# Performance work log

Hardware: AMD Instinct MI355X
Metric: run time of the kernel (lower is better)

## Reference

```python
import math
import jax, jax.numpy as jnp
import numpy as np


def _skew(X, pad_value):
    # shift every row i one step right relative to row i-1: [B,M,L] -> [B,M,M+L]
    B, M, L = X.shape
    X = jnp.pad(X, ((0, 0), (0, 0), (0, M + 1)), constant_values=pad_value)
    X = X.reshape(B, -1)[:, :-M]
    return X.reshape(B, M, M + L)


def _unskew(X):
    # reverse of _skew: [B,M,M+L] -> [B,M,L]
    B, M, ML = X.shape
    L = ML - M
    X = X.reshape(B, -1)
    X = jnp.pad(X, ((0, 0), (0, M)))
    X = X.reshape(B, M, M + L + 1)
    return X[:, :, :L]


def setup_inputs() -> dict:
    key0 = jax.random.key(0)
    k1, k2, k3, k4 = jax.random.split(key0, 4)
    BH, M, D = 64, 1024, 64          # batch*heads, block len, head dim
    L = 1024                          # attn_span
    return {
        "query": jax.random.normal(k1, (BH, M, D), dtype=jnp.float32),
        "key": jax.random.normal(k2, (BH, M + L, D), dtype=jnp.float32),
        "value": jax.random.normal(k3, (BH, M + L, D), dtype=jnp.float32),
        "key_pe": jax.random.normal(k4, (1, D, L), dtype=jnp.float32),
    }


def reference(query, key, value, key_pe):
    hidden_size = query.shape[-1]
    # content scores: [BH, M, M+L] -> banded [BH, M, L]
    attn_cont = _unskew(jnp.matmul(query, jnp.swapaxes(key, -1, -2)))
    # relative position scores: [BH, M, L] (key_pe broadcasts over batch)
    attn_pos = jnp.matmul(query, key_pe)
    attn = (attn_cont + attn_pos) / math.sqrt(hidden_size)
    attn = jax.nn.softmax(attn, axis=-1)
    # dropout p=0.0 -> identity
    attn_skew = _skew(attn, 0.0)          # [BH, M, M+L]
    out = jnp.matmul(attn_skew, value)    # [BH, M, D]
    return out
```

## Files before the change

kernel.cpp:

```cpp
#include <hip/hip_runtime.h>
#include <hip/hip_bf16.h>


typedef __attribute__((ext_vector_type(8))) short bf16x8;
typedef __attribute__((ext_vector_type(4))) short bf16x4;
typedef __attribute__((ext_vector_type(4))) float f32x4;

#define BHN   64
#define MQ    1024
#define DH    64
#define LS    1024
#define NKEY  2048
#define NTILE 17

#define SZ_PE  ((size_t)LS * DH * 2)
#define OFF_K  SZ_PE
#define SZ_K   ((size_t)BHN * NKEY * DH * 2)
#define OFF_V  (OFF_K + SZ_K)
#define SZ_V   ((size_t)BHN * DH * NKEY * 2)
#define WS_NEED (OFF_V + SZ_V)

#define SCL_LOG2E 0.18033688011112042f

__device__ __forceinline__ short f2bf(float f) {
  unsigned u = __float_as_uint(f);
  u += 0x7FFFu + ((u >> 16) & 1u);
  return (short)(u >> 16);
}
__device__ __forceinline__ float bf2f(short s) {
  return __uint_as_float(((unsigned)(unsigned short)s) << 16);
}

#if defined(__has_builtin)
#if __has_builtin(__builtin_amdgcn_cvt_pk_bf16_f32)
#define HAVE_CVT_PK 1
#endif
#if __has_builtin(__builtin_amdgcn_exp2f)
#define HAVE_EXP2 1
#endif
#endif

__device__ __forceinline__ float fast_exp2(float x) {
#ifdef HAVE_EXP2
  return __builtin_amdgcn_exp2f(x);
#else
  return __builtin_exp2f(x);
#endif
}

__device__ __forceinline__ unsigned pk2c(float a, float b) {
  return (unsigned)(unsigned short)f2bf(a) | ((unsigned)(unsigned short)f2bf(b) << 16);
}

__device__ __forceinline__ unsigned pk2a(float a, float b) {
#ifdef HAVE_CVT_PK
  auto r = __builtin_amdgcn_cvt_pk_bf16_f32(a, b);
  unsigned u;
  __builtin_memcpy(&u, &r, 4);
  return u;
#else
  unsigned r;
  asm("v_cvt_pk_bf16_f32 %0, %1, %2" : "=v"(r) : "v"(a), "v"(b));
  return r;
#endif
}
__device__ __forceinline__ bf16x4 mk4(unsigned a, unsigned b) {
  union { unsigned u[2]; bf16x4 v; } z;
  z.u[0] = a; z.u[1] = b;
  return z.v;
}
__device__ __forceinline__ bf16x8 mk8(unsigned a, unsigned b, unsigned c, unsigned d) {
  union { unsigned u[4]; bf16x8 v; } z;
  z.u[0] = a; z.u[1] = b; z.u[2] = c; z.u[3] = d;
  return z.v;
}

__global__ __launch_bounds__(256)
void prep_fused(const float* __restrict__ pe, const float* __restrict__ K,
                const float* __restrict__ V, short* __restrict__ peT,
                short* __restrict__ Kb, short* __restrict__ Vb) {
  __shared__ short st[64 * 68];
  const int bx = blockIdx.x;
  if (bx < 256) {
    const int idx = bx * 256 + threadIdx.x;
    const int rel = idx >> 6, d = idx & 63;
    peT[rel * 64 + (((d >> 3) ^ (rel & 7)) * 8) + (d & 7)] = f2bf(pe[d * LS + rel]);
  } else if (bx < 2304) {
    const size_t i = ((size_t)(bx - 256) * 256 + threadIdx.x) * 16;
    const int row = (int)(i >> 6);
    const int c16 = (int)(i & 63);
    const float4 f0 = *(const float4*)(K + i);
    const float4 f1 = *(const float4*)(K + i + 4);
    const float4 f2 = *(const float4*)(K + i + 8);
    const float4 f3 = *(const float4*)(K + i + 12);
    const bf16x8 b0 = mk8(pk2c(f0.x, f0.y), pk2c(f0.z, f0.w), pk2c(f1.x, f1.y), pk2c(f1.z, f1.w));
    const bf16x8 b1 = mk8(pk2c(f2.x, f2.y), pk2c(f2.z, f2.w), pk2c(f3.x, f3.y), pk2c(f3.z, f3.w));
    const int s7 = row & 7;
    short* dst = Kb + (size_t)row * 64;
    *(bf16x8*)&dst[(((c16 >> 3))     ^ s7) * 8] = b0;
    *(bf16x8*)&dst[(((c16 >> 3) + 1) ^ s7) * 8] = b1;
  } else {
    const int b  = bx - 2304;
    const int bh = b >> 5, jt = b & 31;
    {
      const int r = threadIdx.x >> 2, cb = (threadIdx.x & 3) * 16;
      const float* src = V + ((size_t)bh * NKEY + jt * 64 + r) * DH + cb;
#pragma unroll
      for (int c = 0; c < 16; c += 8) {
        float4 f0 = *(const float4*)(src + c);
        float4 f1 = *(const float4*)(src + c + 4);
        *(bf16x8*)&st[r * 68 + cb + c] =
            mk8(pk2c(f0.x, f0.y), pk2c(f0.z, f0.w), pk2c(f1.x, f1.y), pk2c(f1.z, f1.w));
      }
    }
    __syncthreads();
    {
      const int d = threadIdx.x >> 2, kapb = (threadIdx.x & 3) * 16;
      __attribute__((aligned(16))) short tmp[16];
#pragma unroll
      for (int j = 0; j < 16; ++j) {
        const int kap = kapb + j;
        const int k   = (kap & 3) * 16 + (kap >> 2);
        tmp[j] = st[k * 68 + d];
      }
      short* dst = Vb + ((size_t)bh * DH + d) * NKEY + jt * 64 + kapb;
      *(bf16x8*)dst       = *(bf16x8*)&tmp[0];
      *(bf16x8*)(dst + 8) = *(bf16x8*)&tmp[8];
    }
  }
}

template <bool PRECONV>
__global__ __launch_bounds__(256, 4)
void seq_attn_kernel(const float* __restrict__ Qf, const float* __restrict__ Kf,
                     const float* __restrict__ Vf, const short* __restrict__ peT,
                     const short* __restrict__ Kb, const short* __restrict__ Vb,
                     float* __restrict__ Out) {
  __shared__ short sK[64 * 64];
  __shared__ short sPE[2 * 64 * 64];
  __shared__ short sV[64 * 64];

  const int tid  = threadIdx.x;
  const int w    = tid >> 6;
  const int lane = tid & 63;
  const int li   = lane & 15;
  const int quad = lane >> 4;
  const int linear = blockIdx.y * 16 + blockIdx.x;
  const int slot   = linear >> 3;
  const int bh     = (linear & 7) * 8 + (slot >> 4);
  const int i0     = (slot & 15) * 64;
  const int rbase  = w * 16 + quad * 4;

  bf16x8 aq[2];
  {
    const float* qp = Qf + (size_t)((bh * MQ + i0 + w * 16 + li) * DH) + quad * 8;
#pragma unroll
    for (int ks = 0; ks < 2; ++ks) {
      float4 f0 = *(const float4*)(qp + ks * 32);
      float4 f1 = *(const float4*)(qp + ks * 32 + 4);
      f0.x *= SCL_LOG2E; f0.y *= SCL_LOG2E; f0.z *= SCL_LOG2E; f0.w *= SCL_LOG2E;
      f1.x *= SCL_LOG2E; f1.y *= SCL_LOG2E; f1.z *= SCL_LOG2E; f1.w *= SCL_LOG2E;
      aq[ks] = mk8(pk2a(f0.x, f0.y), pk2a(f0.z, f0.w), pk2a(f1.x, f1.y), pk2a(f1.z, f1.w));
    }
  }

  float l_i[4] = {0.f, 0.f, 0.f, 0.f};
  f32x4 acco[4];
#pragma unroll
  for (int nt = 0; nt < 4; ++nt) acco[nt] = (f32x4){0.f, 0.f, 0.f, 0.f};

  f32x4 curPw[4];
  f32x4 prevw3 = (f32x4){0.f, 0.f, 0.f, 0.f};

  bf16x8 pfK0, pfK1, pfP0, pfP1, pfV0, pfV1;
  const short *pK, *pP, *pV0, *pV1;
  if constexpr (PRECONV) {
    pK = Kb + ((size_t)bh * NKEY + i0) * DH + tid * 8 + 1024;
    pP = peT + tid * 8 + 1024;
    const int d0 = tid >> 3;
    const int g0 = (tid & 7) ^ (d0 & 7);
    pV0 = Vb + ((size_t)bh * DH + d0) * NKEY + i0 + g0 * 8;
    pV1 = pV0 + (size_t)32 * NKEY;
    pfK0 = *(const bf16x8*)(pK - 1024);
    pfK1 = *(const bf16x8*)(pK + 1024);
    pfP0 = *(const bf16x8*)(pP - 1024);
    pfP1 = *(const bf16x8*)(pP + 1024);
    pfV0 = *(const bf16x8*)(pV0);
    pfV1 = *(const bf16x8*)(pV1);
    pK += 4096; pP += 4096; pV0 += 64; pV1 += 64;
  }

  for (int t = 0; t < NTILE; ++t) {
    if constexpr (PRECONV) {
      asm volatile("s_waitcnt lgkmcnt(0)" ::: "memory");
      __builtin_amdgcn_sched_barrier(0);
      __builtin_amdgcn_s_barrier();
      __builtin_amdgcn_sched_barrier(0);
      *(bf16x8*)&sK[tid * 8]        = pfK0;
      *(bf16x8*)&sK[tid * 8 + 2048] = pfK1;
      if (t < NTILE - 1) {
        short* ped = sPE + (size_t)(t & 1) * 4096;
        *(bf16x8*)&ped[tid * 8]        = pfP0;
        *(bf16x8*)&ped[tid * 8 + 2048] = pfP1;
      }
      *(bf16x8*)&sV[tid * 8]        = pfV0;
      *(bf16x8*)&sV[tid * 8 + 2048] = pfV1;
      if (t + 1 < NTILE) {
        pfK0 = *(const bf16x8*)(pK - 1024);
        pfK1 = *(const bf16x8*)(pK + 1024);
        pfV0 = *(const bf16x8*)(pV0);
        pfV1 = *(const bf16x8*)(pV1);
        pK += 4096; pV0 += 64; pV1 += 64;
        if (t + 1 < NTILE - 1) {
          pfP0 = *(const bf16x8*)(pP - 1024);
          pfP1 = *(const bf16x8*)(pP + 1024);
          pP += 4096;
        }
      }
      asm volatile("s_waitcnt lgkmcnt(0)" ::: "memory");
      __builtin_amdgcn_sched_barrier(0);
      __builtin_amdgcn_s_barrier();
      __builtin_amdgcn_sched_barrier(0);
    } else {
      __syncthreads();
      const int j0 = i0 + t * 64;
      {
        const int srow = tid >> 2, l0 = tid & 3, sdb = l0 * 16;
        const float* src = Kf + (size_t)(bh * NKEY + j0 + srow) * DH + sdb;
        const float4 a0 = *(const float4*)(src + 0);
        const float4 a1 = *(const float4*)(src + 4);
        const float4 a2 = *(const float4*)(src + 8);
        const float4 a3 = *(const float4*)(src + 12);
        const bf16x8 b0 = mk8(pk2c(a0.x, a0.y), pk2c(a0.z, a0.w), pk2c(a1.x, a1.y), pk2c(a1.z, a1.w));
        const bf16x8 b1 = mk8(pk2c(a2.x, a2.y), pk2c(a2.z, a2.w), pk2c(a3.x, a3.y), pk2c(a3.z, a3.w));
        const int s7 = srow & 7;
        *(bf16x8*)&sK[srow * 64 + (((2 * l0)     ^ s7) * 8)] = b0;
        *(bf16x8*)&sK[srow * 64 + (((2 * l0 + 1) ^ s7) * 8)] = b1;
      }
      {
        const int vdb = (tid & 15) * 4, vkb = (tid >> 4) * 4;
        const float* src = Vf + (size_t)(bh * NKEY + j0 + vkb) * DH + vdb;
#pragma unroll
        for (int m = 0; m < 4; ++m) {
          const float4 rr = *(const float4*)(src + m * DH);
          const int k   = vkb + m;
          const int kap = (k & 15) * 4 + (k >> 4);
#pragma unroll
          for (int jj = 0; jj < 4; ++jj) {
            const int d = vdb + jj;
            const float fv = (jj == 0) ? rr.x : (jj == 1) ? rr.y : (jj == 2) ? rr.z : rr.w;
            sV[d * 64 + (((kap >> 3) ^ (d & 7)) * 8) + (kap & 7)] = f2bf(fv);
          }
        }
      }
      if (t < NTILE - 1) {
        const short* src = peT + (size_t)t * 64 * 64;
        short* db = sPE + (size_t)(t & 1) * 4096;
        *(bf16x8*)&db[tid * 16]     = *(const bf16x8*)(src + tid * 16);
        *(bf16x8*)&db[tid * 16 + 8] = *(const bf16x8*)(src + tid * 16 + 8);
      }
      __syncthreads();
    }

    __builtin_amdgcn_s_setprio(1);
#pragma unroll
    for (int m = 0; m < 4; ++m) {
      const int colIdx = 4 * t - w + m;
      const int base = ((colIdx >> 2) & 1) * 4096 + ((colIdx & 3) * 16 + li) * 64;
      f32x4 c = (f32x4){0.f, 0.f, 0.f, 0.f};
#pragma unroll
      for (int ks = 0; ks < 2; ++ks) {
        const int gs = (((ks * 4 + quad) ^ (li & 7)) * 8);
        const bf16x8 b = *(bf16x8*)&sPE[base + gs];
        c = __builtin_amdgcn_mfma_f32_16x16x32_bf16(aq[ks], b, c, 0, 0, 0);
      }
      curPw[m] = c;
    }

    f32x4 cs[4];
#pragma unroll
    for (int nt = 0; nt < 4; ++nt) {
      f32x4 c = (f32x4){0.f, 0.f, 0.f, 0.f};
#pragma unroll
      for (int ks = 0; ks < 2; ++ks) {
        const int gs = (((ks * 4 + quad) ^ (li & 7)) * 8);
        const bf16x8 b = *(bf16x8*)&sK[(nt * 16 + li) * 64 + gs];
        c = __builtin_amdgcn_mfma_f32_16x16x32_bf16(aq[ks], b, c, 0, 0, 0);
      }
      cs[nt] = c;
    }
    __builtin_amdgcn_s_setprio(0);

    bf16x4 pkv[4];
#pragma unroll
    for (int r = 0; r < 4; ++r) {
      const int e       = li - quad * 4 - r;
      const bool ge     = (e >= 0);
      const int srcLane = quad * 16 + (e & 15);
      const float shm = __shfl(prevw3[r], srcLane);
      const unsigned pk01 = pk2a(curPw[0][r], curPw[1][r]);
      const unsigned pk23 = pk2a(curPw[2][r], curPw[3][r]);
      const unsigned s01 = (unsigned)__shfl((int)pk01, srcLane);
      const unsigned s23 = (unsigned)__shfl((int)pk23, srcLane);
      const float sh0 = bf2f((short)(s01 & 0xffffu));
      const float sh1 = bf2f((short)(s01 >> 16));
      const float sh2 = bf2f((short)(s23 & 0xffffu));
      const float sh3 = bf2f((short)(s23 >> 16));
      const float pos0 = ge ? sh0 : shm;
      const float pos1 = ge ? sh1 : sh0;
      const float pos2 = ge ? sh2 : sh1;
      const float pos3 = ge ? sh3 : sh2;
      float p0 = fast_exp2(cs[0][r] + pos0);
      float p1 = fast_exp2(cs[1][r] + pos1);
      float p2 = fast_exp2(cs[2][r] + pos2);
      float p3 = fast_exp2(cs[3][r] + pos3);
      if (t == 0) {
        p0 = (0 > w || (0 == w && ge)) ? p0 : 0.f;
        p1 = (1 > w || (1 == w && ge)) ? p1 : 0.f;
        p2 = (2 > w || (2 == w && ge)) ? p2 : 0.f;
        p3 = (3 > w || (3 == w && ge)) ? p3 : 0.f;
      } else if (t == NTILE - 1) {
        p0 = (0 < w || (0 == w && !ge)) ? p0 : 0.f;
        p1 = (1 < w || (1 == w && !ge)) ? p1 : 0.f;
        p2 = (2 < w || (2 == w && !ge)) ? p2 : 0.f;
        p3 = (3 < w || (3 == w && !ge)) ? p3 : 0.f;
      }
      l_i[r] += (p0 + p1) + (p2 + p3);
      pkv[r] = mk4(pk2a(p0, p1), pk2a(p2, p3));
    }
    prevw3 = curPw[3];

    asm volatile("s_waitcnt lgkmcnt(0)" ::: "memory");
    __builtin_amdgcn_sched_barrier(0);
    __builtin_amdgcn_s_barrier();
    __builtin_amdgcn_sched_barrier(0);

#pragma unroll
    for (int r = 0; r < 4; ++r) {
      const int rowA = rbase + r;
      *(bf16x4*)&sK[rowA * 64 + (((li >> 1) ^ (rowA & 7)) * 8) + (li & 1) * 4] = pkv[r];
    }

    __builtin_amdgcn_s_setprio(1);
#pragma unroll
    for (int ks = 0; ks < 2; ++ks) {
      const int rowA = w * 16 + li;
      const bf16x8 ap =
          *(bf16x8*)&sK[rowA * 64 + (((ks * 4 + quad) ^ (rowA & 7)) * 8)];
#pragma unroll
      for (int nt = 0; nt < 4; ++nt) {
        const int d  = nt * 16 + li;
        const int gs = (((ks * 4 + quad) ^ (d & 7)) * 8);
        const bf16x8 bv = *(bf16x8*)&sV[d * 64 + gs];
        acco[nt] = __builtin_amdgcn_mfma_f32_16x16x32_bf16(ap, bv, acco[nt], 0, 0, 0);
      }
    }
    __builtin_amdgcn_s_setprio(0);
  }

#pragma unroll
  for (int r = 0; r < 4; ++r) {
    float l = l_i[r];
    l += __shfl_xor(l, 1);
    l += __shfl_xor(l, 2);
    l += __shfl_xor(l, 4);
    l += __shfl_xor(l, 8);
    const float inv = 1.0f / l;
#pragma unroll
    for (int nt = 0; nt < 4; ++nt) {
      Out[(size_t)(bh * MQ + i0 + rbase + r) * DH + nt * 16 + li] = acco[nt][r] * inv;
    }
  }
}

extern "C" void kernel_launch(void* const* d_in, const int* in_sizes, int n_in,
                              void* d_out, int out_size, void* d_ws, size_t ws_size,
                              hipStream_t stream) {
  const float* q  = (const float*)d_in[0];
  const float* k  = (const float*)d_in[1];
  const float* v  = (const float*)d_in[2];
  const float* pe = (const float*)d_in[3];
  float* out = (float*)d_out;
  short* peT = (short*)d_ws;
  short* Kb  = (short*)((char*)d_ws + OFF_K);
  short* Vb  = (short*)((char*)d_ws + OFF_V);
  const bool preconv = ws_size >= WS_NEED;

  dim3 grid(MQ / 64, BHN);
  if (preconv) {
    prep_fused<<<4352, 256, 0, stream>>>(pe, k, v, peT, Kb, Vb);
    seq_attn_kernel<true><<<grid, 256, 0, stream>>>(q, k, v, peT, Kb, Vb, out);
  } else {
    prep_fused<<<256, 256, 0, stream>>>(pe, k, v, peT, Kb, Vb);
    seq_attn_kernel<false><<<grid, 256, 0, stream>>>(q, k, v, peT, Kb, Vb, out);
  }
}
```

Measured before the change: 165.8 us.

## Double-buffer K/V shared tiles to drop one barrier per iteration

Makes the K and V LDS tiles double-buffered (like PE already was). The next tile is written into the alternate buffer after the PV matmul, so each iteration needs one barrier instead of two around the stores. This raises LDS use to 48KB per block, so launch bounds drop from 4 to 3 blocks per CU, which may reduce occupancy and latency hiding.

Result: slower. 174.4 us (+5.2%).

```diff
diff --git a/kernel.cpp b/kernel.cpp
--- a/kernel.cpp
+++ b/kernel.cpp
@@ -74,6 +74,14 @@
   z.u[0] = a; z.u[1] = b; z.u[2] = c; z.u[3] = d;
   return z.v;
 }
+
+#define RAWBAR()                                          \
+  do {                                                    \
+    asm volatile("s_waitcnt lgkmcnt(0)" ::: "memory");    \
+    __builtin_amdgcn_sched_barrier(0);                    \
+    __builtin_amdgcn_s_barrier();                         \
+    __builtin_amdgcn_sched_barrier(0);                    \
+  } while (0)
 
 __global__ __launch_bounds__(256)
 void prep_fused(const float* __restrict__ pe, const float* __restrict__ K,
@@ -131,14 +139,14 @@
 }
 
 template <bool PRECONV>
-__global__ __launch_bounds__(256, 4)
+__global__ __launch_bounds__(256, 3)
 void seq_attn_kernel(const float* __restrict__ Qf, const float* __restrict__ Kf,
                      const float* __restrict__ Vf, const short* __restrict__ peT,
                      const short* __restrict__ Kb, const short* __restrict__ Vb,
                      float* __restrict__ Out) {
-  __shared__ short sK[64 * 64];
+  __shared__ short sK[2 * 64 * 64];
   __shared__ short sPE[2 * 64 * 64];
-  __shared__ short sV[64 * 64];
+  __shared__ short sV[2 * 64 * 64];
 
   const int tid  = threadIdx.x;
   const int w    = tid >> 6;
@@ -188,40 +196,26 @@
     pfV0 = *(const bf16x8*)(pV0);
     pfV1 = *(const bf16x8*)(pV1);
     pK += 4096; pP += 4096; pV0 += 64; pV1 += 64;
+    *(bf16x8*)&sK[tid * 8]         = pfK0;
+    *(bf16x8*)&sK[tid * 8 + 2048]  = pfK1;
+    *(bf16x8*)&sPE[tid * 8]        = pfP0;
+    *(bf16x8*)&sPE[tid * 8 + 2048] = pfP1;
+    *(bf16x8*)&sV[tid * 8]         = pfV0;
+    *(bf16x8*)&sV[tid * 8 + 2048]  = pfV1;
+    pfK0 = *(const bf16x8*)(pK - 1024);
+    pfK1 = *(const bf16x8*)(pK + 1024);
+    pfP0 = *(const bf16x8*)(pP - 1024);
+    pfP1 = *(const bf16x8*)(pP + 1024);
+    pfV0 = *(const bf16x8*)(pV0);
+    pfV1 = *(const bf16x8*)(pV1);
+    pK += 4096; pP += 4096; pV0 += 64; pV1 += 64;
+    RAWBAR();
   }
 
   for (int t = 0; t < NTILE; ++t) {
-    if constexpr (PRECONV) {
-      asm volatile("s_waitcnt lgkmcnt(0)" ::: "memory");
-      __builtin_amdgcn_sched_barrier(0);
-      __builtin_amdgcn_s_barrier();
-      __builtin_amdgcn_sched_barrier(0);
-      *(bf16x8*)&sK[tid * 8]        = pfK0;
-      *(bf16x8*)&sK[tid * 8 + 2048] = pfK1;
-      if (t < NTILE - 1) {
-        short* ped = sPE + (size_t)(t & 1) * 4096;
-        *(bf16x8*)&ped[tid * 8]        = pfP0;
-        *(bf16x8*)&ped[tid * 8 + 2048] = pfP1;
-      }
-      *(bf16x8*)&sV[tid * 8]        = pfV0;
-      *(bf16x8*)&sV[tid * 8 + 2048] = pfV1;
-      if (t + 1 < NTILE) {
-        pfK0 = *(const bf16x8*)(pK - 1024);
-        pfK1 = *(const bf16x8*)(pK + 1024);
-        pfV0 = *(const bf16x8*)(pV0);
-        pfV1 = *(const bf16x8*)(pV1);
-        pK += 4096; pV0 += 64; pV1 += 64;
-        if (t + 1 < NTILE - 1) {
-          pfP0 = *(const bf16x8*)(pP - 1024);
-          pfP1 = *(const bf16x8*)(pP + 1024);
-          pP += 4096;
-        }
-      }
-      asm volatile("s_waitcnt lgkmcnt(0)" ::: "memory");
-      __builtin_amdgcn_sched_barrier(0);
-      __builtin_amdgcn_s_barrier();
-      __builtin_amdgcn_sched_barrier(0);
-    } else {
+    const int cb = PRECONV ? ((t & 1) * 4096) : 0;
+
+    if constexpr (!PRECONV) {
       __syncthreads();
       const int j0 = i0 + t * 64;
       {
@@ -284,7 +278,7 @@
 #pragma unroll
       for (int ks = 0; ks < 2; ++ks) {
         const int gs = (((ks * 4 + quad) ^ (li & 7)) * 8);
-        const bf16x8 b = *(bf16x8*)&sK[(nt * 16 + li) * 64 + gs];
+        const bf16x8 b = *(bf16x8*)&sK[cb + (nt * 16 + li) * 64 + gs];
         c = __builtin_amdgcn_mfma_f32_16x16x32_bf16(aq[ks], b, c, 0, 0, 0);
       }
       cs[nt] = c;
@@ -338,7 +332,7 @@
 #pragma unroll
     for (int r = 0; r < 4; ++r) {
       const int rowA = rbase + r;
-      *(bf16x4*)&sK[rowA * 64 + (((li >> 1) ^ (rowA & 7)) * 8) + (li & 1) * 4] = pkv[r];
+      *(bf16x4*)&sK[cb + rowA * 64 + (((li >> 1) ^ (rowA & 7)) * 8) + (li & 1) * 4] = pkv[r];
     }
 
     __builtin_amdgcn_s_setprio(1);
@@ -346,16 +340,44 @@
     for (int ks = 0; ks < 2; ++ks) {
       const int rowA = w * 16 + li;
       const bf16x8 ap =
-          *(bf16x8*)&sK[rowA * 64 + (((ks * 4 + quad) ^ (rowA & 7)) * 8)];
+          *(bf16x8*)&sK[cb + rowA * 64 + (((ks * 4 + quad) ^ (rowA & 7)) * 8)];
 #pragma unroll
       for (int nt = 0; nt < 4; ++nt) {
         const int d  = nt * 16 + li;
         const int gs = (((ks * 4 + quad) ^ (d & 7)) * 8);
-        const bf16x8 bv = *(bf16x8*)&sV[d * 64 + gs];
+        const bf16x8 bv = *(bf16x8*)&sV[cb + d * 64 + gs];
         acco[nt] = __builtin_amdgcn_mfma_f32_16x16x32_bf16(ap, bv, acco[nt], 0, 0, 0);
       }
     }
     __builtin_amdgcn_s_setprio(0);
+
+    if constexpr (PRECONV) {
+      if (t + 1 < NTILE) {
+        const int nb = ((t + 1) & 1) * 4096;
+        *(bf16x8*)&sK[nb + tid * 8]        = pfK0;
+        *(bf16x8*)&sK[nb + tid * 8 + 2048] = pfK1;
+        if (t + 1 < NTILE - 1) {
+          short* ped = sPE + (size_t)((t + 1) & 1) * 4096;
+          *(bf16x8*)&ped[tid * 8]        = pfP0;
+          *(bf16x8*)&ped[tid * 8 + 2048] = pfP1;
+        }
+        *(bf16x8*)&sV[nb + tid * 8]        = pfV0;
+        *(bf16x8*)&sV[nb + tid * 8 + 2048] = pfV1;
+        if (t + 2 < NTILE) {
+          pfK0 = *(const bf16x8*)(pK - 1024);
+          pfK1 = *(const bf16x8*)(pK + 1024);
+          pfV0 = *(const bf16x8*)(pV0);
+          pfV1 = *(const bf16x8*)(pV1);
+          pK += 4096; pV0 += 64; pV1 += 64;
+          if (t + 2 < NTILE - 1) {
+            pfP0 = *(const bf16x8*)(pP - 1024);
+            pfP1 = *(const bf16x8*)(pP + 1024);
+            pP += 4096;
+          }
+        }
+        RAWBAR();
+      }
+    }
   }
 
 #pragma unroll
```
